# Performance work log

Measured on AMD Instinct MI355X. Metric: run time of the kernel, lower is better.

Reference implementation:

```python
import jax, jax.numpy as jnp
import numpy as np

L = 3          # num_gc_layers
DIM = 128      # hidden dim (== num_features)
BN_EPS = 1e-5


def _bn(h, gamma, beta):
    # torch BatchNorm1d training-mode normalization (biased variance)
    m = h.mean(axis=0)
    v = h.var(axis=0)
    return gamma * (h - m) * jax.lax.rsqrt(v + BN_EPS) + beta


def setup_inputs() -> dict:
    key = jax.random.key(0)
    ks = jax.random.split(key, 24)
    N, E, G = 50000, 600000, 256
    s = 0.05
    inp = {
        "x": jax.random.normal(ks[0], (N, DIM), jnp.float32),
        "src": jax.random.randint(ks[1], (E,), 0, N, jnp.int32),
        "dst": jax.random.randint(ks[2], (E,), 0, N, jnp.int32),
        "batch": jnp.sort(jax.random.randint(ks[3], (N,), 0, G, jnp.int32)),
        "n_graphs": G,
        # GIN MLP params (stacked over layers; num_features == dim)
        "conv_w1": jax.random.normal(ks[4], (L, DIM, DIM), jnp.float32) * s,
        "conv_b1": jnp.zeros((L, DIM), jnp.float32),
        "conv_w2": jax.random.normal(ks[5], (L, DIM, DIM), jnp.float32) * s,
        "conv_b2": jnp.zeros((L, DIM), jnp.float32),
        "bn_gamma": jnp.ones((L, DIM), jnp.float32),
        "bn_beta": jnp.zeros((L, DIM), jnp.float32),
        # summary weighter (dim -> 1)
        "sw_w": jax.random.normal(ks[6], (DIM, 1), jnp.float32) * s,
        "sw_b": jnp.zeros((1,), jnp.float32),
        # VAE heads
        "nmu_w": jax.random.normal(ks[7], (DIM, DIM), jnp.float32) * s,
        "nmu_b": jnp.zeros((DIM,), jnp.float32),
        "nlv_w": jax.random.normal(ks[8], (DIM, DIM), jnp.float32) * s,
        "nlv_b": jnp.zeros((DIM,), jnp.float32),
        "gmu_w": jax.random.normal(ks[9], (DIM, DIM), jnp.float32) * s,
        "gmu_b": jnp.zeros((DIM,), jnp.float32),
        "glv_w": jax.random.normal(ks[10], (DIM, DIM), jnp.float32) * s,
        "glv_b": jnp.zeros((DIM,), jnp.float32),
        # head BN params, order: [node_mu, node_logvar, graph_mu, graph_logvar]
        "head_gamma": jnp.ones((4, DIM), jnp.float32),
        "head_beta": jnp.zeros((4, DIM), jnp.float32),
    }
    return inp


def reference(x, src, dst, batch, n_graphs,
              conv_w1, conv_b1, conv_w2, conv_b2, bn_gamma, bn_beta,
              sw_w, sw_b, nmu_w, nmu_b, nlv_w, nlv_b,
              gmu_w, gmu_b, glv_w, glv_b, head_gamma, head_beta):
    N = x.shape[0]
    for i in range(L):
        # GINConv (eps=0): h = nn(x + sum_{j->i} x_j)
        agg = jax.ops.segment_sum(x[src], dst, num_segments=N)  # [N, dim]
        h = x + agg
        h = jax.nn.relu(h @ conv_w1[i] + conv_b1[i]) @ conv_w2[i] + conv_b2[i]
        x = _bn(jax.nn.relu(h), bn_gamma[i], bn_beta[i])

    w = jax.nn.sigmoid(x @ sw_w + sw_b)           # [N, 1]
    summary_info = w * x                          # [N, dim]
    noisy_info = (1.0 - w) * x                    # [N, dim]
    slots = jax.ops.segment_sum(summary_info, batch, num_segments=n_graphs)  # [G, dim]

    node_mu = _bn(jax.nn.relu(noisy_info @ nmu_w + nmu_b), head_gamma[0], head_beta[0])
    node_logvar = _bn(jax.nn.relu(noisy_info @ nlv_w + nlv_b), head_gamma[1], head_beta[1])
    graph_mu = _bn(jax.nn.relu(slots @ gmu_w + gmu_b), head_gamma[2], head_beta[2])
    graph_logvar = _bn(jax.nn.relu(slots @ glv_w + glv_b), head_gamma[3], head_beta[3])
    return (node_mu, node_logvar, graph_mu, graph_logvar)
```

## Files before the change

kernel.cpp:

```cpp
#include <hip/hip_runtime.h>
#include <hip/hip_bf16.h>

#define DIM 128
#define BN_EPS 1e-5f
#define NSTRIPE 32

typedef unsigned short ushortT;
typedef __attribute__((ext_vector_type(8))) short short8;
typedef __attribute__((ext_vector_type(4))) float floatx4;

__device__ __forceinline__ float bflo(unsigned u) { return __uint_as_float(u << 16); }
__device__ __forceinline__ float bfhi(unsigned u) { return __uint_as_float(u & 0xffff0000u); }
__device__ __forceinline__ float bf2f(ushortT h) { return __uint_as_float(((unsigned)h) << 16); }
__device__ __forceinline__ ushortT f2bf(float f) {
    unsigned x = __float_as_uint(f);
    unsigned r = (x + 0x7fff + ((x >> 16) & 1)) >> 16;
    return (ushortT)r;
}
__device__ __forceinline__ void decode8(const unsigned* ap, short8& hi, short8& lo) {
#pragma unroll
    for (int j = 0; j < 8; ++j) {
        hi[j] = (short)(ap[j] >> 16);
        lo[j] = (short)(ap[j] & 0xffffu);
    }
}
__device__ __forceinline__ void acc8(float* a, uint4 v) {
    a[0] += bflo(v.x); a[1] += bfhi(v.x);
    a[2] += bflo(v.y); a[3] += bfhi(v.y);
    a[4] += bflo(v.z); a[5] += bfhi(v.z);
    a[6] += bflo(v.w); a[7] += bfhi(v.w);
}

__global__ __launch_bounds__(256) void hist_kernel(
    const int* __restrict__ dst, int* __restrict__ deg, int E)
{
    int e = blockIdx.x * 256 + threadIdx.x;
    if (e < E) atomicAdd(&deg[dst[e]], 1);
}

__global__ __launch_bounds__(256) void scan1_kernel(
    const int* __restrict__ deg, int* __restrict__ iscan,
    int* __restrict__ bsum, int N)
{
    __shared__ int s[256];
    int t = threadIdx.x;
    int i = blockIdx.x * 256 + t;
    int v = (i < N) ? deg[i] : 0;
    s[t] = v;
    __syncthreads();
#pragma unroll
    for (int off = 1; off < 256; off <<= 1) {
        int u = (t >= off) ? s[t - off] : 0;
        __syncthreads();
        s[t] += u;
        __syncthreads();
    }
    if (i < N) iscan[i] = s[t];
    if (t == 255) bsum[blockIdx.x] = s[255];
}

__global__ __launch_bounds__(256) void scan2_kernel(int* __restrict__ bsum, int nb)
{
    __shared__ int s[256];
    int t = threadIdx.x;
    int v = (t < nb) ? bsum[t] : 0;
    s[t] = v;
    __syncthreads();
#pragma unroll
    for (int off = 1; off < 256; off <<= 1) {
        int u = (t >= off) ? s[t - off] : 0;
        __syncthreads();
        s[t] += u;
        __syncthreads();
    }
    if (t < nb) bsum[t] = s[t] - v;
}

__global__ __launch_bounds__(256) void scan3_kernel(
    const int* __restrict__ iscan, const int* __restrict__ bsum,
    const int* __restrict__ deg, int* __restrict__ row_ptr,
    int* __restrict__ cur, int N)
{
    int i = blockIdx.x * 256 + threadIdx.x;
    if (i < N) {
        int inc = iscan[i] + bsum[i >> 8];
        row_ptr[i + 1] = inc;
        cur[i] = inc - deg[i];
    }
    if (i == 0) row_ptr[0] = 0;
}

__global__ __launch_bounds__(256) void fill_kernel(
    const int* __restrict__ src, const int* __restrict__ dst,
    int* __restrict__ cur, int* __restrict__ eidx, int E)
{
    int e = blockIdx.x * 256 + threadIdx.x;
    if (e < E) {
        int pos = atomicAdd(&cur[dst[e]], 1);
        eidx[pos] = src[e];
    }
}

__global__ __launch_bounds__(256) void prep_kernel(
    const float* __restrict__ cw1, const float* __restrict__ cw2,
    const float* __restrict__ nmu, const float* __restrict__ nlv,
    const float* __restrict__ gmu, const float* __restrict__ glv,
    ushortT* __restrict__ whi, ushortT* __restrict__ wlo,
    const float* __restrict__ x, ushortT* __restrict__ xb, int n8, int cxBlocks,
    float4* __restrict__ zsbuf, int sbufQ,
    float4* __restrict__ zslots, int slotsQ,
    float4* __restrict__ zdeg, int degQ,
    float4* __restrict__ zstats, int statsQ)
{
    int b = blockIdx.x, t = threadIdx.x;
    if (b < 640) {
        int tid = b * 256 + t;
        int mat = tid >> 14;
        int i   = tid & 16383;
        int n = i >> 7, k = i & 127;
        const float* Wm = (mat < 3) ? cw1 + (size_t)mat * 16384
                        : (mat < 6) ? cw2 + (size_t)(mat - 3) * 16384
                        : (mat == 6) ? nmu : (mat == 7) ? nlv
                        : (mat == 8) ? gmu : glv;
        float w = Wm[k * DIM + n];
        ushortT h = f2bf(w);
        whi[(size_t)mat * 16384 + i] = h;
        wlo[(size_t)mat * 16384 + i] = f2bf(w - bf2f(h));
    } else if (b < 640 + cxBlocks) {
        int i = (b - 640) * 256 + t;
        if (i < n8) {
            const float4* xp = (const float4*)x;
            float4 a = xp[2 * i], bb = xp[2 * i + 1];
            uint4 o;
            o.x = (unsigned)f2bf(a.x) | ((unsigned)f2bf(a.y) << 16);
            o.y = (unsigned)f2bf(a.z) | ((unsigned)f2bf(a.w) << 16);
            o.z = (unsigned)f2bf(bb.x) | ((unsigned)f2bf(bb.y) << 16);
            o.w = (unsigned)f2bf(bb.z) | ((unsigned)f2bf(bb.w) << 16);
            ((uint4*)xb)[i] = o;
        }
    } else {
        int q = (b - 640 - cxBlocks) * 256 + t;
        float4 z = make_float4(0.f, 0.f, 0.f, 0.f);
        if (q < sbufQ) zsbuf[q] = z;
        else if ((q -= sbufQ) < slotsQ) zslots[q] = z;
        else if ((q -= slotsQ) < degQ) zdeg[q] = z;
        else if ((q -= degQ) < statsQ) zstats[q] = z;
    }
}

__global__ __launch_bounds__(256) void layer_fused_kernel(
    const ushortT* __restrict__ Xb, const int* __restrict__ row_ptr,
    const int* __restrict__ eidx,
    const float* __restrict__ sprev,
    const float* __restrict__ gamma, const float* __restrict__ beta,
    const ushortT* __restrict__ W1hi, const ushortT* __restrict__ W1lo,
    const float* __restrict__ b1,
    const ushortT* __restrict__ W2hi, const ushortT* __restrict__ W2lo,
    const float* __restrict__ b2,
    ushortT* __restrict__ rout, float* __restrict__ sdst,
    int M, float invM)
{
    __shared__ unsigned As[32][DIM + 4];
    __shared__ float ls[DIM], lsq[DIM];
    __shared__ float pstat[256];
    int t = threadIdx.x;
    int wave = t >> 6, lane = t & 63, quad = lane >> 4, l16 = lane & 15;
    int m0 = blockIdx.x * 32;

    if (sprev) {
        float s = 0.f;
#pragma unroll
        for (int i = 0; i < NSTRIPE; ++i) s += sprev[i * 256 + t];
        pstat[t] = s;
    }
    if (t < DIM) { ls[t] = 0.f; lsq[t] = 0.f; }
    __syncthreads();

    {
        int nloc = t >> 3;
        int c0   = (t & 7) * 16;
        int node = m0 + nloc;
        float acc[16];
#pragma unroll
        for (int j = 0; j < 16; ++j) acc[j] = 0.f;
        if (node < M) {
            int b = row_ptr[node];
            int e = row_ptr[node + 1];
            const ushortT* xrow = Xb + (size_t)node * DIM + c0;
            acc8(&acc[0], *(const uint4*)(xrow));
            acc8(&acc[8], *(const uint4*)(xrow + 8));
            int i = b;
            for (; i + 4 <= e; i += 4) {
                int s0 = eidx[i], s1 = eidx[i + 1], s2 = eidx[i + 2], s3 = eidx[i + 3];
                const ushortT* p0 = Xb + (size_t)s0 * DIM + c0;
                const ushortT* p1 = Xb + (size_t)s1 * DIM + c0;
                const ushortT* p2 = Xb + (size_t)s2 * DIM + c0;
                const ushortT* p3 = Xb + (size_t)s3 * DIM + c0;
                uint4 v00 = *(const uint4*)(p0), v01 = *(const uint4*)(p0 + 8);
                uint4 v10 = *(const uint4*)(p1), v11 = *(const uint4*)(p1 + 8);
                uint4 v20 = *(const uint4*)(p2), v21 = *(const uint4*)(p2 + 8);
                uint4 v30 = *(const uint4*)(p3), v31 = *(const uint4*)(p3 + 8);
                acc8(&acc[0], v00); acc8(&acc[8], v01);
                acc8(&acc[0], v10); acc8(&acc[8], v11);
                acc8(&acc[0], v20); acc8(&acc[8], v21);
                acc8(&acc[0], v30); acc8(&acc[8], v31);
            }
            for (; i < e; ++i) {
                const ushortT* sp = Xb + (size_t)eidx[i] * DIM + c0;
                acc8(&acc[0], *(const uint4*)(sp));
                acc8(&acc[8], *(const uint4*)(sp + 8));
            }
            if (sprev) {
                float cnt = (float)(e - b + 1);
#pragma unroll
                for (int jq = 0; jq < 4; ++jq) {
                    int c = c0 + jq * 4;
                    float4 sm = *(const float4*)&pstat[c];
                    float4 sq = *(const float4*)&pstat[128 + c];
                    float4 gm = *(const float4*)(gamma + c);
                    float4 bt = *(const float4*)(beta + c);
                    float m, sc;
                    m = sm.x * invM; sc = gm.x * rsqrtf(sq.x * invM - m * m + BN_EPS);
                    acc[jq * 4 + 0] = sc * acc[jq * 4 + 0] + cnt * (bt.x - sc * m);
                    m = sm.y * invM; sc = gm.y * rsqrtf(sq.y * invM - m * m + BN_EPS);
                    acc[jq * 4 + 1] = sc * acc[jq * 4 + 1] + cnt * (bt.y - sc * m);
                    m = sm.z * invM; sc = gm.z * rsqrtf(sq.z * invM - m * m + BN_EPS);
                    acc[jq * 4 + 2] = sc * acc[jq * 4 + 2] + cnt * (bt.z - sc * m);
                    m = sm.w * invM; sc = gm.w * rsqrtf(sq.w * invM - m * m + BN_EPS);
                    acc[jq * 4 + 3] = sc * acc[jq * 4 + 3] + cnt * (bt.w - sc * m);
                }
            }
        }
        unsigned pk[16];
#pragma unroll
        for (int j = 0; j < 16; ++j) {
            ushortT h = f2bf(acc[j]);
            ushortT l = f2bf(acc[j] - bf2f(h));
            pk[j] = ((unsigned)h << 16) | l;
        }
#pragma unroll
        for (int j4 = 0; j4 < 4; ++j4)
            *(uint4*)&As[nloc][c0 + j4 * 4] = *(uint4*)&pk[j4 * 4];
    }
    __syncthreads();

    int cbase = wave * 32;
    floatx4 acc[2][2];
#pragma unroll
    for (int mt = 0; mt < 2; ++mt)
#pragma unroll
        for (int nt = 0; nt < 2; ++nt)
            acc[mt][nt] = (floatx4){0.f, 0.f, 0.f, 0.f};

#pragma unroll
    for (int ks = 0; ks < 4; ++ks) {
        int k0 = ks * 32 + quad * 8;
        short8 bhi[2], blo[2];
#pragma unroll
        for (int nt = 0; nt < 2; ++nt) {
            const size_t woff = (size_t)(cbase + nt * 16 + l16) * DIM + k0;
            bhi[nt] = *(const short8*)(W1hi + woff);
            blo[nt] = *(const short8*)(W1lo + woff);
        }
#pragma unroll
        for (int mt = 0; mt < 2; ++mt) {
            int lr = mt * 16 + l16;
            unsigned ap[8];
            *(uint4*)&ap[0] = *(const uint4*)&As[lr][k0];
            *(uint4*)&ap[4] = *(const uint4*)&As[lr][k0 + 4];
            short8 ahi, alo;
            decode8(ap, ahi, alo);
#pragma unroll
            for (int nt = 0; nt < 2; ++nt) {
                acc[mt][nt] = __builtin_amdgcn_mfma_f32_16x16x32_bf16(ahi, bhi[nt], acc[mt][nt], 0, 0, 0);
                acc[mt][nt] = __builtin_amdgcn_mfma_f32_16x16x32_bf16(alo, bhi[nt], acc[mt][nt], 0, 0, 0);
                acc[mt][nt] = __builtin_amdgcn_mfma_f32_16x16x32_bf16(ahi, blo[nt], acc[mt][nt], 0, 0, 0);
            }
        }
    }
    __syncthreads();

#pragma unroll
    for (int nt = 0; nt < 2; ++nt) {
        int col = cbase + nt * 16 + l16;
        float bcol = b1[col];
#pragma unroll
        for (int mt = 0; mt < 2; ++mt)
#pragma unroll
            for (int r = 0; r < 4; ++r) {
                int lr = mt * 16 + quad * 4 + r;
                float v = fmaxf(acc[mt][nt][r] + bcol, 0.f);
                ushortT hv = f2bf(v);
                ushortT lv = f2bf(v - bf2f(hv));
                As[lr][col] = ((unsigned)hv << 16) | lv;
            }
    }
    __syncthreads();

#pragma unroll
    for (int mt = 0; mt < 2; ++mt)
#pragma unroll
        for (int nt = 0; nt < 2; ++nt)
            acc[mt][nt] = (floatx4){0.f, 0.f, 0.f, 0.f};

#pragma unroll
    for (int ks = 0; ks < 4; ++ks) {
        int k0 = ks * 32 + quad * 8;
        short8 bhi[2], blo[2];
#pragma unroll
        for (int nt = 0; nt < 2; ++nt) {
            const size_t woff = (size_t)(cbase + nt * 16 + l16) * DIM + k0;
            bhi[nt] = *(const short8*)(W2hi + woff);
            blo[nt] = *(const short8*)(W2lo + woff);
        }
#pragma unroll
        for (int mt = 0; mt < 2; ++mt) {
            int lr = mt * 16 + l16;
            unsigned ap[8];
            *(uint4*)&ap[0] = *(const uint4*)&As[lr][k0];
            *(uint4*)&ap[4] = *(const uint4*)&As[lr][k0 + 4];
            short8 ahi, alo;
            decode8(ap, ahi, alo);
#pragma unroll
            for (int nt = 0; nt < 2; ++nt) {
                acc[mt][nt] = __builtin_amdgcn_mfma_f32_16x16x32_bf16(ahi, bhi[nt], acc[mt][nt], 0, 0, 0);
                acc[mt][nt] = __builtin_amdgcn_mfma_f32_16x16x32_bf16(alo, bhi[nt], acc[mt][nt], 0, 0, 0);
                acc[mt][nt] = __builtin_amdgcn_mfma_f32_16x16x32_bf16(ahi, blo[nt], acc[mt][nt], 0, 0, 0);
            }
        }
    }
#pragma unroll
    for (int nt = 0; nt < 2; ++nt) {
        int col = cbase + nt * 16 + l16;
        float bcol = b2[col];
        float s = 0.f, sq = 0.f;
#pragma unroll
        for (int mt = 0; mt < 2; ++mt)
#pragma unroll
            for (int r = 0; r < 4; ++r) {
                int gr = m0 + mt * 16 + quad * 4 + r;
                if (gr < M) {
                    float v = fmaxf(acc[mt][nt][r] + bcol, 0.f);
                    rout[(size_t)gr * DIM + col] = f2bf(v);
                    s += v;
                    sq += v * v;
                }
            }
        s  += __shfl_xor(s, 16);  s  += __shfl_xor(s, 32);
        sq += __shfl_xor(sq, 16); sq += __shfl_xor(sq, 32);
        if (quad == 0) {
            atomicAdd(&ls[col], s);
            atomicAdd(&lsq[col], sq);
        }
    }
    __syncthreads();
    float* dstp = sdst + (size_t)(blockIdx.x & (NSTRIPE - 1)) * 256;
    if (t < 128) atomicAdd(&dstp[t], ls[t]);
    else         atomicAdd(&dstp[t], lsq[t - 128]);
}

__global__ __launch_bounds__(256) void weigh_heads_kernel(
    const ushortT* __restrict__ R, const int* __restrict__ batch,
    const float* __restrict__ sprev,
    const float* __restrict__ gamma, const float* __restrict__ beta,
    const float* __restrict__ sw_w, const float* __restrict__ sw_b,
    float* __restrict__ slots,
    const ushortT* __restrict__ WAhi, const ushortT* __restrict__ WAlo,
    const float* __restrict__ bA, ushortT* __restrict__ hA, float* __restrict__ sdstA,
    const ushortT* __restrict__ WBhi, const ushortT* __restrict__ WBlo,
    const float* __restrict__ bB, ushortT* __restrict__ hB, float* __restrict__ sdstB,
    int N, float invM)
{
    __shared__ unsigned As[64][DIM + 4];
    __shared__ float pstat[256];
    __shared__ float part[256];
    __shared__ float wsh[64];
    __shared__ float lsA[DIM], lsqA[DIM], lsB[DIM], lsqB[DIM];
    int t = threadIdx.x;
    int wave = t >> 6, lane = t & 63, quad = lane >> 4, l16 = lane & 15;
    int m0 = blockIdx.x * 64;

    {
        float s = 0.f;
#pragma unroll
        for (int i = 0; i < NSTRIPE; ++i) s += sprev[i * 256 + t];
        pstat[t] = s;
    }
    if (t < DIM) { lsA[t] = 0.f; lsqA[t] = 0.f; lsB[t] = 0.f; lsqB[t] = 0.f; }
    __syncthreads();

    {
        int row = m0 + (t >> 2);
        int cs  = (t & 3) * 32;
        float d = 0.f;
        if (row < N) {
            for (int c = cs; c < cs + 32; c += 4) {
                uint2 u = *(const uint2*)(R + (size_t)row * DIM + c);
                float rv[4] = {bflo(u.x), bfhi(u.x), bflo(u.y), bfhi(u.y)};
                float4 sm = *(const float4*)&pstat[c];
                float4 sq = *(const float4*)&pstat[128 + c];
                float4 gm = *(const float4*)(gamma + c);
                float4 bt = *(const float4*)(beta + c);
                float4 sw = *(const float4*)(sw_w + c);
                float m, sc;
                m = sm.x * invM; sc = gm.x * rsqrtf(sq.x * invM - m * m + BN_EPS);
                d += (sc * (rv[0] - m) + bt.x) * sw.x;
                m = sm.y * invM; sc = gm.y * rsqrtf(sq.y * invM - m * m + BN_EPS);
                d += (sc * (rv[1] - m) + bt.y) * sw.y;
                m = sm.z * invM; sc = gm.z * rsqrtf(sq.z * invM - m * m + BN_EPS);
                d += (sc * (rv[2] - m) + bt.z) * sw.z;
                m = sm.w * invM; sc = gm.w * rsqrtf(sq.w * invM - m * m + BN_EPS);
                d += (sc * (rv[3] - m) + bt.w) * sw.w;
            }
        }
        part[t] = d;
    }
    __syncthreads();
    if (t < 64) {
        float dd = part[4 * t] + part[4 * t + 1] + part[4 * t + 2] + part[4 * t + 3];
        wsh[t] = 1.0f / (1.0f + expf(-(dd + sw_b[0])));
    }
    __syncthreads();

    {
        int c    = t & 127;
        int half = t >> 7;
        float m   = pstat[c] * invM;
        float var = pstat[128 + c] * invM - m * m;
        float sc  = gamma[c] * rsqrtf(var + BN_EPS);
        float sh  = beta[c] - sc * m;
        int curg = -1;
        float acc = 0.f;
        for (int r = half; r < 64; r += 2) {
            int row = m0 + r;
            if (row < N) {
                float xv = sc * bf2f(R[(size_t)row * DIM + c]) + sh;
                float w  = wsh[r];
                float nv = (1.f - w) * xv;
                ushortT hv = f2bf(nv);
                ushortT lv = f2bf(nv - bf2f(hv));
                As[r][c] = ((unsigned)hv << 16) | lv;
                int g = batch[row];
                if (g != curg) {
                    if (curg >= 0) atomicAdd(&slots[(size_t)curg * DIM + c], acc);
                    curg = g;
                    acc = 0.f;
                }
                acc += w * xv;
            } else {
                As[r][c] = 0;
            }
        }
        if (curg >= 0) atomicAdd(&slots[(size_t)curg * DIM + c], acc);
    }
    __syncthreads();

    int cbase = wave * 32;
    floatx4 accA[4][2], accB[4][2];
#pragma unroll
    for (int mt = 0; mt < 4; ++mt)
#pragma unroll
        for (int nt = 0; nt < 2; ++nt) {
            accA[mt][nt] = (floatx4){0.f, 0.f, 0.f, 0.f};
            accB[mt][nt] = (floatx4){0.f, 0.f, 0.f, 0.f};
        }

    for (int ks = 0; ks < 4; ++ks) {
        int k0 = ks * 32 + quad * 8;
        short8 bAhi[2], bAlo[2], bBhi[2], bBlo[2];
#pragma unroll
        for (int nt = 0; nt < 2; ++nt) {
            const size_t woff = (size_t)(cbase + nt * 16 + l16) * DIM + k0;
            bAhi[nt] = *(const short8*)(WAhi + woff);
            bAlo[nt] = *(const short8*)(WAlo + woff);
            bBhi[nt] = *(const short8*)(WBhi + woff);
            bBlo[nt] = *(const short8*)(WBlo + woff);
        }
#pragma unroll
        for (int mt = 0; mt < 4; ++mt) {
            int lr = mt * 16 + l16;
            unsigned ap[8];
            *(uint4*)&ap[0] = *(const uint4*)&As[lr][k0];
            *(uint4*)&ap[4] = *(const uint4*)&As[lr][k0 + 4];
            short8 ahi, alo;
            decode8(ap, ahi, alo);
#pragma unroll
            for (int nt = 0; nt < 2; ++nt) {
                accA[mt][nt] = __builtin_amdgcn_mfma_f32_16x16x32_bf16(ahi, bAhi[nt], accA[mt][nt], 0, 0, 0);
                accA[mt][nt] = __builtin_amdgcn_mfma_f32_16x16x32_bf16(alo, bAhi[nt], accA[mt][nt], 0, 0, 0);
                accA[mt][nt] = __builtin_amdgcn_mfma_f32_16x16x32_bf16(ahi, bAlo[nt], accA[mt][nt], 0, 0, 0);
                accB[mt][nt] = __builtin_amdgcn_mfma_f32_16x16x32_bf16(ahi, bBhi[nt], accB[mt][nt], 0, 0, 0);
                accB[mt][nt] = __builtin_amdgcn_mfma_f32_16x16x32_bf16(alo, bBhi[nt], accB[mt][nt], 0, 0, 0);
                accB[mt][nt] = __builtin_amdgcn_mfma_f32_16x16x32_bf16(ahi, bBlo[nt], accB[mt][nt], 0, 0, 0);
            }
        }
    }

#pragma unroll
    for (int nt = 0; nt < 2; ++nt) {
        int col = cbase + nt * 16 + l16;
        float bcA = bA[col], bcB = bB[col];
        float sA = 0.f, sqA = 0.f, sB = 0.f, sqB = 0.f;
#pragma unroll
        for (int mt = 0; mt < 4; ++mt)
#pragma unroll
            for (int r = 0; r < 4; ++r) {
                int gr = m0 + mt * 16 + quad * 4 + r;
                if (gr < N) {
                    size_t off = (size_t)gr * DIM + col;
                    float vA = fmaxf(accA[mt][nt][r] + bcA, 0.f);
                    float vB = fmaxf(accB[mt][nt][r] + bcB, 0.f);
                    hA[off] = f2bf(vA);
                    hB[off] = f2bf(vB);
                    sA += vA; sqA += vA * vA;
                    sB += vB; sqB += vB * vB;
                }
            }
        sA += __shfl_xor(sA, 16);  sA += __shfl_xor(sA, 32);
        sqA += __shfl_xor(sqA, 16); sqA += __shfl_xor(sqA, 32);
        sB += __shfl_xor(sB, 16);  sB += __shfl_xor(sB, 32);
        sqB += __shfl_xor(sqB, 16); sqB += __shfl_xor(sqB, 32);
        if (quad == 0) {
            atomicAdd(&lsA[col], sA);
            atomicAdd(&lsqA[col], sqA);
            atomicAdd(&lsB[col], sB);
            atomicAdd(&lsqB[col], sqB);
        }
    }
    __syncthreads();
    int stripe = blockIdx.x & (NSTRIPE - 1);
    float* dA = sdstA + (size_t)stripe * 256;
    float* dB = sdstB + (size_t)stripe * 256;
    if (t < 128) { atomicAdd(&dA[t], lsA[t]); atomicAdd(&dB[t], lsB[t]); }
    else         { atomicAdd(&dA[t], lsqA[t - 128]); atomicAdd(&dB[t], lsqB[t - 128]); }
}

__global__ __launch_bounds__(256) void merge_stats2_kernel(
    const float* __restrict__ sA, float* __restrict__ oA,
    const float* __restrict__ sB, float* __restrict__ oB)
{
    const float* s = blockIdx.x ? sB : sA;
    float* o = blockIdx.x ? oB : oA;
    int t = threadIdx.x;
    float v = 0.f;
#pragma unroll
    for (int i = 0; i < NSTRIPE; ++i) v += s[i * 256 + t];
    o[t] = v;
}

__global__ __launch_bounds__(256) void gemm_graph_dual_kernel(
    const float* __restrict__ A32,
    const ushortT* __restrict__ W8hi, const ushortT* __restrict__ W8lo,
    const float* __restrict__ b8, float* __restrict__ C8, float* __restrict__ st8,
    const ushortT* __restrict__ W9hi, const ushortT* __restrict__ W9lo,
    const float* __restrict__ b9, float* __restrict__ C9, float* __restrict__ st9,
    int M, int nb)
{
    __shared__ float ls[DIM], lsq[DIM];
    int bb = blockIdx.x;
    const ushortT* Whi; const ushortT* Wlo; const float* bias; float* C; float* st;
    if (bb < nb) { Whi = W8hi; Wlo = W8lo; bias = b8; C = C8; st = st8; }
    else { bb -= nb; Whi = W9hi; Wlo = W9lo; bias = b9; C = C9; st = st9; }

    int t     = threadIdx.x;
    int wave  = t >> 6;
    int lane  = t & 63;
    int quad  = lane >> 4;
    int l16   = lane & 15;
    int m0    = bb * 64;
    int cbase = wave * 32;

    if (t < DIM) { ls[t] = 0.f; lsq[t] = 0.f; }
    __syncthreads();

    floatx4 acc[4][2];
#pragma unroll
    for (int mt = 0; mt < 4; ++mt)
#pragma unroll
        for (int nt = 0; nt < 2; ++nt)
            acc[mt][nt] = (floatx4){0.f, 0.f, 0.f, 0.f};

    for (int ks = 0; ks < 4; ++ks) {
        int k0 = ks * 32 + quad * 8;
        short8 bhi[2], blo[2];
#pragma unroll
        for (int nt = 0; nt < 2; ++nt) {
            const size_t woff = (size_t)(cbase + nt * 16 + l16) * DIM + k0;
            bhi[nt] = *(const short8*)(Whi + woff);
            blo[nt] = *(const short8*)(Wlo + woff);
        }
#pragma unroll
        for (int mt = 0; mt < 4; ++mt) {
            int row = m0 + mt * 16 + l16;
            short8 ahi = {0,0,0,0,0,0,0,0};
            short8 alo = {0,0,0,0,0,0,0,0};
            if (row < M) {
                float av[8];
                *(float4*)&av[0] = *(const float4*)(A32 + (size_t)row * DIM + k0);
                *(float4*)&av[4] = *(const float4*)(A32 + (size_t)row * DIM + k0 + 4);
#pragma unroll
                for (int j = 0; j < 8; ++j) {
                    ushortT hv = f2bf(av[j]);
                    ahi[j] = (short)hv;
                    alo[j] = (short)f2bf(av[j] - bf2f(hv));
                }
            }
#pragma unroll
            for (int nt = 0; nt < 2; ++nt) {
                acc[mt][nt] = __builtin_amdgcn_mfma_f32_16x16x32_bf16(ahi, bhi[nt], acc[mt][nt], 0, 0, 0);
                acc[mt][nt] = __builtin_amdgcn_mfma_f32_16x16x32_bf16(alo, bhi[nt], acc[mt][nt], 0, 0, 0);
                acc[mt][nt] = __builtin_amdgcn_mfma_f32_16x16x32_bf16(ahi, blo[nt], acc[mt][nt], 0, 0, 0);
            }
        }
    }

#pragma unroll
    for (int nt = 0; nt < 2; ++nt) {
        int col = cbase + nt * 16 + l16;
        float bcol = bias[col];
        float s = 0.f, sq = 0.f;
#pragma unroll
        for (int mt = 0; mt < 4; ++mt)
#pragma unroll
            for (int r = 0; r < 4; ++r) {
                int gr = m0 + mt * 16 + quad * 4 + r;
                if (gr < M) {
                    float v = fmaxf(acc[mt][nt][r] + bcol, 0.f);
                    C[(size_t)gr * DIM + col] = v;
                    s += v;
                    sq += v * v;
                }
            }
        s  += __shfl_xor(s, 16);  s  += __shfl_xor(s, 32);
        sq += __shfl_xor(sq, 16); sq += __shfl_xor(sq, 32);
        if (quad == 0) {
            atomicAdd(&ls[col], s);
            atomicAdd(&lsq[col], sq);
        }
    }
    __syncthreads();
    if (t < DIM) {
        atomicAdd(&st[t], ls[t]);
        atomicAdd(&st[DIM + t], lsq[t]);
    }
}

__global__ __launch_bounds__(256) void bn_dual_bf16_kernel(
    const ushortT* __restrict__ RA, float* __restrict__ OA, const float* __restrict__ stA,
    const float* __restrict__ gA, const float* __restrict__ bA,
    const ushortT* __restrict__ RB, float* __restrict__ OB, const float* __restrict__ stB,
    const float* __restrict__ gB, const float* __restrict__ bB,
    int M, int nb)
{
    int bb = blockIdx.x;
    const ushortT* R; float* O; const float* st; const float* gamma; const float* beta;
    if (bb < nb) { R = RA; O = OA; st = stA; gamma = gA; beta = bA; }
    else { bb -= nb; R = RB; O = OB; st = stB; gamma = gB; beta = bB; }
    int idx = bb * 256 + threadIdx.x;
    if (idx >= M * 32) return;
    int c4 = idx & 31;
    float invM = 1.0f / (float)M;
    uint2 u = ((const uint2*)R)[idx];
    float o[4] = {bflo(u.x), bfhi(u.x), bflo(u.y), bfhi(u.y)};
#pragma unroll
    for (int j = 0; j < 4; ++j) {
        int c = c4 * 4 + j;
        float m   = st[c] * invM;
        float var = st[DIM + c] * invM - m * m;
        float sc  = gamma[c] * rsqrtf(var + BN_EPS);
        o[j] = sc * (o[j] - m) + beta[c];
    }
    ((float4*)O)[idx] = make_float4(o[0], o[1], o[2], o[3]);
}

__global__ __launch_bounds__(256) void bn_dual_f32_kernel(
    float* __restrict__ CA, const float* __restrict__ stA,
    const float* __restrict__ gA, const float* __restrict__ bA,
    float* __restrict__ CB, const float* __restrict__ stB,
    const float* __restrict__ gB, const float* __restrict__ bB,
    int M, int nb)
{
    int bb = blockIdx.x;
    float* C; const float* st; const float* gamma; const float* beta;
    if (bb < nb) { C = CA; st = stA; gamma = gA; beta = bA; }
    else { bb -= nb; C = CB; st = stB; gamma = gB; beta = bB; }
    int idx = bb * 256 + threadIdx.x;
    if (idx >= M * 32) return;
    int c4 = idx & 31;
    float invM = 1.0f / (float)M;
    float4 v = ((const float4*)C)[idx];
    float o[4] = {v.x, v.y, v.z, v.w};
#pragma unroll
    for (int j = 0; j < 4; ++j) {
        int c = c4 * 4 + j;
        float m   = st[c] * invM;
        float var = st[DIM + c] * invM - m * m;
        float sc  = gamma[c] * rsqrtf(var + BN_EPS);
        o[j] = sc * (o[j] - m) + beta[c];
    }
    ((float4*)C)[idx] = make_float4(o[0], o[1], o[2], o[3]);
}

extern "C" void kernel_launch(void* const* d_in, const int* in_sizes, int n_in,
                              void* d_out, int out_size, void* d_ws, size_t ws_size,
                              hipStream_t stream)
{
    const float* x      = (const float*)d_in[0];
    const int*   src    = (const int*)d_in[1];
    const int*   dst    = (const int*)d_in[2];
    const int*   batch  = (const int*)d_in[3];
    const float* cw1    = (const float*)d_in[5];
    const float* cb1    = (const float*)d_in[6];
    const float* cw2    = (const float*)d_in[7];
    const float* cb2    = (const float*)d_in[8];
    const float* bng    = (const float*)d_in[9];
    const float* bnb    = (const float*)d_in[10];
    const float* sw_w   = (const float*)d_in[11];
    const float* sw_b   = (const float*)d_in[12];
    const float* nmu_b  = (const float*)d_in[14];
    const float* nlv_b  = (const float*)d_in[16];
    const float* gmu_b  = (const float*)d_in[18];
    const float* glv_b  = (const float*)d_in[20];
    const float* hgam   = (const float*)d_in[21];
    const float* hbet   = (const float*)d_in[22];
    const float* nmu_w  = (const float*)d_in[13];
    const float* nlv_w  = (const float*)d_in[15];
    const float* gmu_w  = (const float*)d_in[17];
    const float* glv_w  = (const float*)d_in[19];

    const int N = in_sizes[0] / DIM;
    const int E = in_sizes[1];
    const int G = (out_size / DIM - 2 * N) / 2;

    float* out0 = (float*)d_out;
    float* out1 = out0 + (size_t)N * DIM;
    float* out2 = out1 + (size_t)N * DIM;
    float* out3 = out2 + (size_t)G * DIM;

    char* wp = (char*)d_ws;
    auto alloc = [&](size_t bytes) {
        char* p = wp;
        wp += (bytes + 255) & ~(size_t)255;
        return p;
    };
    ushortT*  xbf   = (ushortT*)alloc((size_t)N * DIM * 2);
    ushortT*  rA    = (ushortT*)alloc((size_t)N * DIM * 2);
    ushortT*  rB    = (ushortT*)alloc((size_t)N * DIM * 2);
    unsigned* noisyP= (unsigned*)alloc((size_t)N * DIM * 4);
    ushortT*  whi   = (ushortT*)alloc((size_t)10 * 16384 * 2);
    ushortT*  wlo   = (ushortT*)alloc((size_t)10 * 16384 * 2);
    float* slots    = (float*)alloc((size_t)G * DIM * 4);
    float* stats    = (float*)alloc((size_t)7 * 256 * 4);
    float* sbuf     = (float*)alloc((size_t)5 * NSTRIPE * 256 * 4);
    int* row_ptr    = (int*)alloc((size_t)(N + 2) * 4);
    int* eidx       = (int*)alloc((size_t)E * 4);
    int* deg   = (int*)noisyP;
    int* iscan = deg + N;
    int* bsum  = iscan + N;
    int* cur   = bsum + 256;

    auto SS = [&](int i) { return stats + (size_t)i * 256; };
    auto SB = [&](int i) { return sbuf + (size_t)i * NSTRIPE * 256; };

    const int edge_blocks  = (E + 255) / 256;
    const int scan_blocks  = (N + 255) / 256;
    const int layer_blocks = (N + 31) / 32;
    const int heads_blocks = (N + 63) / 64;
    const int g16_blocks   = (N * 16 + 255) / 256;
    const int g32_blocks   = (N * 32 + 255) / 256;
    const float invN = 1.0f / (float)N;

    const int sbufQ  = (5 * NSTRIPE * 256) / 4;
    const int slotsQ = (G * DIM) / 4;
    const int degQ   = (N + 3) / 4;
    const int statsQ = (7 * 256) / 4;
    const int zeroQ  = sbufQ + slotsQ + degQ + statsQ;
    const int zero_blocks = (zeroQ + 255) / 256;

    prep_kernel<<<640 + g16_blocks + zero_blocks, 256, 0, stream>>>(
        cw1, cw2, nmu_w, nlv_w, gmu_w, glv_w, whi, wlo,
        x, xbf, N * 16, g16_blocks,
        (float4*)sbuf, sbufQ, (float4*)slots, slotsQ,
        (float4*)deg, degQ, (float4*)stats, statsQ);

    hist_kernel<<<edge_blocks, 256, 0, stream>>>(dst, deg, E);
    scan1_kernel<<<scan_blocks, 256, 0, stream>>>(deg, iscan, bsum, N);
    scan2_kernel<<<1, 256, 0, stream>>>(bsum, scan_blocks);
    scan3_kernel<<<scan_blocks, 256, 0, stream>>>(iscan, bsum, deg, row_ptr, cur, N);
    fill_kernel<<<edge_blocks, 256, 0, stream>>>(src, dst, cur, eidx, E);

    const ushortT* lin[3]  = {xbf, rA, rB};
    ushortT*       lout[3] = {rA, rB, rA};
    for (int l = 0; l < 3; ++l) {
        const float* sprev  = (l == 0) ? nullptr : SB(l - 1);
        const float* g_prev = (l == 0) ? nullptr : bng + (size_t)(l - 1) * DIM;
        const float* b_prev = (l == 0) ? nullptr : bnb + (size_t)(l - 1) * DIM;
        layer_fused_kernel<<<layer_blocks, 256, 0, stream>>>(
            lin[l], row_ptr, eidx,
            sprev, g_prev, b_prev,
            whi + (size_t)l * 16384, wlo + (size_t)l * 16384, cb1 + (size_t)l * DIM,
            whi + (size_t)(3 + l) * 16384, wlo + (size_t)(3 + l) * 16384, cb2 + (size_t)l * DIM,
            lout[l], SB(l), N, invN);
    }
    ushortT* rfin = rA;
    ushortT* hA   = rB;
    ushortT* hB   = xbf;

    weigh_heads_kernel<<<heads_blocks, 256, 0, stream>>>(
        rfin, batch, SB(2), bng + 2 * DIM, bnb + 2 * DIM,
        sw_w, sw_b, slots,
        whi + (size_t)6 * 16384, wlo + (size_t)6 * 16384, nmu_b, hA, SB(3),
        whi + (size_t)7 * 16384, wlo + (size_t)7 * 16384, nlv_b, hB, SB(4),
        N, invN);
    merge_stats2_kernel<<<2, 256, 0, stream>>>(SB(3), SS(3), SB(4), SS(4));
    bn_dual_bf16_kernel<<<2 * g32_blocks, 256, 0, stream>>>(
        hA, out0, SS(3), hgam + 0 * DIM, hbet + 0 * DIM,
        hB, out1, SS(4), hgam + 1 * DIM, hbet + 1 * DIM, N, g32_blocks);

    const int gemm_blocks_G = (G + 63) / 64;
    const int gbn_blocks    = (G * 32 + 255) / 256;
    gemm_graph_dual_kernel<<<2 * gemm_blocks_G, 256, 0, stream>>>(
        slots,
        whi + (size_t)8 * 16384, wlo + (size_t)8 * 16384, gmu_b, out2, SS(5),
        whi + (size_t)9 * 16384, wlo + (size_t)9 * 16384, glv_b, out3, SS(6),
        G, gemm_blocks_G);
    bn_dual_f32_kernel<<<2 * gbn_blocks, 256, 0, stream>>>(
        out2, SS(5), hgam + 2 * DIM, hbet + 2 * DIM,
        out3, SS(6), hgam + 3 * DIM, hbet + 3 * DIM, G, gbn_blocks);
}
```

Before: 455.0 us.

## Cut launch count: atomic-offset CSR alloc, fuse stats merge and graph BN

Replaces the three-kernel prefix scan with a single kernel that reserves each block's segment through an atomic counter, so rows are no longer globally ordered and each row is described by a start plus its degree. The stats merge is folded into the node-head BN kernel, which now runs as a fixed grid-stride launch. The graph-head BN is applied by the last finishing block of the graph GEMM, detected with a counter. Together these remove several small launches and their serialization, at the cost of non-deterministic edge ordering and a tail done by one block.

```diff
diff --git a/kernel.cpp b/kernel.cpp
--- a/kernel.cpp
+++ b/kernel.cpp
@@ -38,11 +38,12 @@
     if (e < E) atomicAdd(&deg[dst[e]], 1);
 }
 
-__global__ __launch_bounds__(256) void scan1_kernel(
-    const int* __restrict__ deg, int* __restrict__ iscan,
-    int* __restrict__ bsum, int N)
+__global__ __launch_bounds__(256) void alloc_kernel(
+    const int* __restrict__ deg, int* __restrict__ rstart,
+    int* __restrict__ cur, int* __restrict__ total, int N)
 {
     __shared__ int s[256];
+    __shared__ int base;
     int t = threadIdx.x;
     int i = blockIdx.x * 256 + t;
     int v = (i < N) ? deg[i] : 0;
@@ -55,39 +56,13 @@
         s[t] += u;
         __syncthreads();
     }
-    if (i < N) iscan[i] = s[t];
-    if (t == 255) bsum[blockIdx.x] = s[255];
-}
-
-__global__ __launch_bounds__(256) void scan2_kernel(int* __restrict__ bsum, int nb)
-{
-    __shared__ int s[256];
-    int t = threadIdx.x;
-    int v = (t < nb) ? bsum[t] : 0;
-    s[t] = v;
-    __syncthreads();
-#pragma unroll
-    for (int off = 1; off < 256; off <<= 1) {
-        int u = (t >= off) ? s[t - off] : 0;
-        __syncthreads();
-        s[t] += u;
-        __syncthreads();
-    }
-    if (t < nb) bsum[t] = s[t] - v;
-}
-
-__global__ __launch_bounds__(256) void scan3_kernel(
-    const int* __restrict__ iscan, const int* __restrict__ bsum,
-    const int* __restrict__ deg, int* __restrict__ row_ptr,
-    int* __restrict__ cur, int N)
-{
-    int i = blockIdx.x * 256 + threadIdx.x;
+    if (t == 255) base = atomicAdd(total, s[255]);
+    __syncthreads();
     if (i < N) {
-        int inc = iscan[i] + bsum[i >> 8];
-        row_ptr[i + 1] = inc;
-        cur[i] = inc - deg[i];
-    }
-    if (i == 0) row_ptr[0] = 0;
+        int pos = base + s[t] - v;
+        rstart[i] = pos;
+        cur[i] = pos;
+    }
 }
 
 __global__ __launch_bounds__(256) void fill_kernel(
@@ -149,8 +124,8 @@
 }
 
 __global__ __launch_bounds__(256) void layer_fused_kernel(
-    const ushortT* __restrict__ Xb, const int* __restrict__ row_ptr,
-    const int* __restrict__ eidx,
+    const ushortT* __restrict__ Xb, const int* __restrict__ rstart,
+    const int* __restrict__ degp, const int* __restrict__ eidx,
     const float* __restrict__ sprev,
     const float* __restrict__ gamma, const float* __restrict__ beta,
     const ushortT* __restrict__ W1hi, const ushortT* __restrict__ W1lo,
@@ -184,8 +159,9 @@
 #pragma unroll
         for (int j = 0; j < 16; ++j) acc[j] = 0.f;
         if (node < M) {
-            int b = row_ptr[node];
-            int e = row_ptr[node + 1];
+            int b = rstart[node];
+            int dg = degp[node];
+            int e = b + dg;
             const ushortT* xrow = Xb + (size_t)node * DIM + c0;
             acc8(&acc[0], *(const uint4*)(xrow));
             acc8(&acc[8], *(const uint4*)(xrow + 8));
@@ -211,7 +187,7 @@
                 acc8(&acc[8], *(const uint4*)(sp + 8));
             }
             if (sprev) {
-                float cnt = (float)(e - b + 1);
+                float cnt = (float)(dg + 1);
 #pragma unroll
                 for (int jq = 0; jq < 4; ++jq) {
                     int c = c0 + jq * 4;
@@ -535,32 +511,67 @@
     else         { atomicAdd(&dA[t], lsqA[t - 128]); atomicAdd(&dB[t], lsqB[t - 128]); }
 }
 
-__global__ __launch_bounds__(256) void merge_stats2_kernel(
-    const float* __restrict__ sA, float* __restrict__ oA,
-    const float* __restrict__ sB, float* __restrict__ oB)
+__global__ __launch_bounds__(256) void bn_dual_bf16_kernel(
+    const ushortT* __restrict__ RA, float* __restrict__ OA, const float* __restrict__ sbA,
+    const float* __restrict__ gA, const float* __restrict__ bA,
+    const ushortT* __restrict__ RB, float* __restrict__ OB, const float* __restrict__ sbB,
+    const float* __restrict__ gB, const float* __restrict__ bB,
+    int M, int nbh)
 {
-    const float* s = blockIdx.x ? sB : sA;
-    float* o = blockIdx.x ? oB : oA;
+    __shared__ float pstat[256];
+    __shared__ float scL[128], shL[128];
+    int bb = blockIdx.x;
+    const ushortT* R; float* O; const float* sb; const float* gamma; const float* beta;
+    if (bb < nbh) { R = RA; O = OA; sb = sbA; gamma = gA; beta = bA; }
+    else { bb -= nbh; R = RB; O = OB; sb = sbB; gamma = gB; beta = bB; }
     int t = threadIdx.x;
-    float v = 0.f;
-#pragma unroll
-    for (int i = 0; i < NSTRIPE; ++i) v += s[i * 256 + t];
-    o[t] = v;
-}
-
-__global__ __launch_bounds__(256) void gemm_graph_dual_kernel(
+    {
+        float s = 0.f;
+#pragma unroll
+        for (int i = 0; i < NSTRIPE; ++i) s += sb[i * 256 + t];
+        pstat[t] = s;
+    }
+    __syncthreads();
+    float invM = 1.0f / (float)M;
+    if (t < 128) {
+        float m   = pstat[t] * invM;
+        float var = pstat[128 + t] * invM - m * m;
+        float sc  = gamma[t] * rsqrtf(var + BN_EPS);
+        scL[t] = sc;
+        shL[t] = beta[t] - sc * m;
+    }
+    __syncthreads();
+    int Q = M * 32;
+    for (int idx = bb * 256 + t; idx < Q; idx += nbh * 256) {
+        int c4 = idx & 31;
+        uint2 u = ((const uint2*)R)[idx];
+        float o[4] = {bflo(u.x), bfhi(u.x), bflo(u.y), bfhi(u.y)};
+#pragma unroll
+        for (int j = 0; j < 4; ++j) {
+            int c = c4 * 4 + j;
+            o[j] = scL[c] * o[j] + shL[c];
+        }
+        ((float4*)O)[idx] = make_float4(o[0], o[1], o[2], o[3]);
+    }
+}
+
+__global__ __launch_bounds__(256) void gemm_graph_dual_bn_kernel(
     const float* __restrict__ A32,
     const ushortT* __restrict__ W8hi, const ushortT* __restrict__ W8lo,
     const float* __restrict__ b8, float* __restrict__ C8, float* __restrict__ st8,
+    const float* __restrict__ g8, const float* __restrict__ be8, int* __restrict__ cnt8,
     const ushortT* __restrict__ W9hi, const ushortT* __restrict__ W9lo,
     const float* __restrict__ b9, float* __restrict__ C9, float* __restrict__ st9,
+    const float* __restrict__ g9, const float* __restrict__ be9, int* __restrict__ cnt9,
     int M, int nb)
 {
     __shared__ float ls[DIM], lsq[DIM];
+    __shared__ int lastB;
     int bb = blockIdx.x;
     const ushortT* Whi; const ushortT* Wlo; const float* bias; float* C; float* st;
-    if (bb < nb) { Whi = W8hi; Wlo = W8lo; bias = b8; C = C8; st = st8; }
-    else { bb -= nb; Whi = W9hi; Wlo = W9lo; bias = b9; C = C9; st = st9; }
+    const float* gamma; const float* beta; int* cnt;
+    if (bb < nb) { Whi = W8hi; Wlo = W8lo; bias = b8; C = C8; st = st8; gamma = g8; beta = be8; cnt = cnt8; }
+    else { bb -= nb; Whi = W9hi; Wlo = W9lo; bias = b9; C = C9; st = st9; gamma = g9; beta = be9; cnt = cnt9; }
 
     int t     = threadIdx.x;
     int wave  = t >> 6;
@@ -643,62 +654,27 @@
         atomicAdd(&st[t], ls[t]);
         atomicAdd(&st[DIM + t], lsq[t]);
     }
-}
-
-__global__ __launch_bounds__(256) void bn_dual_bf16_kernel(
-    const ushortT* __restrict__ RA, float* __restrict__ OA, const float* __restrict__ stA,
-    const float* __restrict__ gA, const float* __restrict__ bA,
-    const ushortT* __restrict__ RB, float* __restrict__ OB, const float* __restrict__ stB,
-    const float* __restrict__ gB, const float* __restrict__ bB,
-    int M, int nb)
-{
-    int bb = blockIdx.x;
-    const ushortT* R; float* O; const float* st; const float* gamma; const float* beta;
-    if (bb < nb) { R = RA; O = OA; st = stA; gamma = gA; beta = bA; }
-    else { bb -= nb; R = RB; O = OB; st = stB; gamma = gB; beta = bB; }
-    int idx = bb * 256 + threadIdx.x;
-    if (idx >= M * 32) return;
-    int c4 = idx & 31;
-    float invM = 1.0f / (float)M;
-    uint2 u = ((const uint2*)R)[idx];
-    float o[4] = {bflo(u.x), bfhi(u.x), bflo(u.y), bfhi(u.y)};
-#pragma unroll
-    for (int j = 0; j < 4; ++j) {
-        int c = c4 * 4 + j;
-        float m   = st[c] * invM;
-        float var = st[DIM + c] * invM - m * m;
-        float sc  = gamma[c] * rsqrtf(var + BN_EPS);
-        o[j] = sc * (o[j] - m) + beta[c];
-    }
-    ((float4*)O)[idx] = make_float4(o[0], o[1], o[2], o[3]);
-}
-
-__global__ __launch_bounds__(256) void bn_dual_f32_kernel(
-    float* __restrict__ CA, const float* __restrict__ stA,
-    const float* __restrict__ gA, const float* __restrict__ bA,
-    float* __restrict__ CB, const float* __restrict__ stB,
-    const float* __restrict__ gB, const float* __restrict__ bB,
-    int M, int nb)
-{
-    int bb = blockIdx.x;
-    float* C; const float* st; const float* gamma; const float* beta;
-    if (bb < nb) { C = CA; st = stA; gamma = gA; beta = bA; }
-    else { bb -= nb; C = CB; st = stB; gamma = gB; beta = bB; }
-    int idx = bb * 256 + threadIdx.x;
-    if (idx >= M * 32) return;
-    int c4 = idx & 31;
-    float invM = 1.0f / (float)M;
-    float4 v = ((const float4*)C)[idx];
-    float o[4] = {v.x, v.y, v.z, v.w};
-#pragma unroll
-    for (int j = 0; j < 4; ++j) {
-        int c = c4 * 4 + j;
-        float m   = st[c] * invM;
-        float var = st[DIM + c] * invM - m * m;
-        float sc  = gamma[c] * rsqrtf(var + BN_EPS);
-        o[j] = sc * (o[j] - m) + beta[c];
-    }
-    ((float4*)C)[idx] = make_float4(o[0], o[1], o[2], o[3]);
+    __threadfence();
+    if (t == 0) lastB = (atomicAdd(cnt, 1) == nb - 1) ? 1 : 0;
+    __syncthreads();
+    if (lastB) {
+        __threadfence();
+        float invG = 1.0f / (float)M;
+        for (int idx = t; idx < M * 32; idx += 256) {
+            int c4 = idx & 31;
+            float4 v = ((const float4*)C)[idx];
+            float o[4] = {v.x, v.y, v.z, v.w};
+#pragma unroll
+            for (int j = 0; j < 4; ++j) {
+                int c = c4 * 4 + j;
+                float m   = st[c] * invG;
+                float var = st[DIM + c] * invG - m * m;
+                float sc  = gamma[c] * rsqrtf(var + BN_EPS);
+                o[j] = sc * (o[j] - m) + beta[c];
+            }
+            ((float4*)C)[idx] = make_float4(o[0], o[1], o[2], o[3]);
+        }
+    }
 }
 
 extern "C" void kernel_launch(void* const* d_in, const int* in_sizes, int n_in,
@@ -750,30 +726,32 @@
     ushortT*  whi   = (ushortT*)alloc((size_t)10 * 16384 * 2);
     ushortT*  wlo   = (ushortT*)alloc((size_t)10 * 16384 * 2);
     float* slots    = (float*)alloc((size_t)G * DIM * 4);
-    float* stats    = (float*)alloc((size_t)7 * 256 * 4);
+    float* stats    = (float*)alloc((size_t)8 * 256 * 4);
     float* sbuf     = (float*)alloc((size_t)5 * NSTRIPE * 256 * 4);
-    int* row_ptr    = (int*)alloc((size_t)(N + 2) * 4);
+    int* rstart     = (int*)alloc((size_t)(N + 2) * 4);
     int* eidx       = (int*)alloc((size_t)E * 4);
     int* deg   = (int*)noisyP;
     int* iscan = deg + N;
     int* bsum  = iscan + N;
     int* cur   = bsum + 256;
-
-    auto SS = [&](int i) { return stats + (size_t)i * 256; };
+    (void)iscan; (void)bsum;
+
     auto SB = [&](int i) { return sbuf + (size_t)i * NSTRIPE * 256; };
+    float* SS5 = stats + (size_t)5 * 256;
+    float* SS6 = stats + (size_t)6 * 256;
+    int*   cnts = (int*)(stats + (size_t)7 * 256);
 
     const int edge_blocks  = (E + 255) / 256;
     const int scan_blocks  = (N + 255) / 256;
     const int layer_blocks = (N + 31) / 32;
     const int heads_blocks = (N + 63) / 64;
     const int g16_blocks   = (N * 16 + 255) / 256;
-    const int g32_blocks   = (N * 32 + 255) / 256;
     const float invN = 1.0f / (float)N;
 
     const int sbufQ  = (5 * NSTRIPE * 256) / 4;
     const int slotsQ = (G * DIM) / 4;
     const int degQ   = (N + 3) / 4;
-    const int statsQ = (7 * 256) / 4;
+    const int statsQ = (8 * 256) / 4;
     const int zeroQ  = sbufQ + slotsQ + degQ + statsQ;
     const int zero_blocks = (zeroQ + 255) / 256;
 
@@ -784,9 +762,7 @@
         (float4*)deg, degQ, (float4*)stats, statsQ);
 
     hist_kernel<<<edge_blocks, 256, 0, stream>>>(dst, deg, E);
-    scan1_kernel<<<scan_blocks, 256, 0, stream>>>(deg, iscan, bsum, N);
-    scan2_kernel<<<1, 256, 0, stream>>>(bsum, scan_blocks);
-    scan3_kernel<<<scan_blocks, 256, 0, stream>>>(iscan, bsum, deg, row_ptr, cur, N);
+    alloc_kernel<<<scan_blocks, 256, 0, stream>>>(deg, rstart, cur, cnts, N);
     fill_kernel<<<edge_blocks, 256, 0, stream>>>(src, dst, cur, eidx, E);
 
     const ushortT* lin[3]  = {xbf, rA, rB};
@@ -796,7 +772,7 @@
         const float* g_prev = (l == 0) ? nullptr : bng + (size_t)(l - 1) * DIM;
         const float* b_prev = (l == 0) ? nullptr : bnb + (size_t)(l - 1) * DIM;
         layer_fused_kernel<<<layer_blocks, 256, 0, stream>>>(
-            lin[l], row_ptr, eidx,
+            lin[l], rstart, deg, eidx,
             sprev, g_prev, b_prev,
             whi + (size_t)l * 16384, wlo + (size_t)l * 16384, cb1 + (size_t)l * DIM,
             whi + (size_t)(3 + l) * 16384, wlo + (size_t)(3 + l) * 16384, cb2 + (size_t)l * DIM,
@@ -812,19 +788,18 @@
         whi + (size_t)6 * 16384, wlo + (size_t)6 * 16384, nmu_b, hA, SB(3),
         whi + (size_t)7 * 16384, wlo + (size_t)7 * 16384, nlv_b, hB, SB(4),
         N, invN);
-    merge_stats2_kernel<<<2, 256, 0, stream>>>(SB(3), SS(3), SB(4), SS(4));
-    bn_dual_bf16_kernel<<<2 * g32_blocks, 256, 0, stream>>>(
-        hA, out0, SS(3), hgam + 0 * DIM, hbet + 0 * DIM,
-        hB, out1, SS(4), hgam + 1 * DIM, hbet + 1 * DIM, N, g32_blocks);
+
+    const int bn_nbh = 256;
+    bn_dual_bf16_kernel<<<2 * bn_nbh, 256, 0, stream>>>(
+        hA, out0, SB(3), hgam + 0 * DIM, hbet + 0 * DIM,
+        hB, out1, SB(4), hgam + 1 * DIM, hbet + 1 * DIM, N, bn_nbh);
 
     const int gemm_blocks_G = (G + 63) / 64;
-    const int gbn_blocks    = (G * 32 + 255) / 256;
-    gemm_graph_dual_kernel<<<2 * gemm_blocks_G, 256, 0, stream>>>(
+    gemm_graph_dual_bn_kernel<<<2 * gemm_blocks_G, 256, 0, stream>>>(
         slots,
-        whi + (size_t)8 * 16384, wlo + (size_t)8 * 16384, gmu_b, out2, SS(5),
-        whi + (size_t)9 * 16384, wlo + (size_t)9 * 16384, glv_b, out3, SS(6),
+        whi + (size_t)8 * 16384, wlo + (size_t)8 * 16384, gmu_b, out2, SS5,
+        hgam + 2 * DIM, hbet + 2 * DIM, cnts + 1,
+        whi + (size_t)9 * 16384, wlo + (size_t)9 * 16384, glv_b, out3, SS6,
+        hgam + 3 * DIM, hbet + 3 * DIM, cnts + 2,
         G, gemm_blocks_G);
-    bn_dual_f32_kernel<<<2 * gbn_blocks, 256, 0, stream>>>(
-        out2, SS(5), hgam + 2 * DIM, hbet + 2 * DIM,
-        out3, SS(6), hgam + 3 * DIM, hbet + 3 * DIM, G, gbn_blocks);
-}
+}
```

After: 461.8 us. No clear change (+1.5%).
